# Kernel optimization log

Measured on AMD Instinct MI355X. Metric: run time of the kernel, lower is better.

## Reference

```python
import jax, jax.numpy as jnp
import numpy as np

N_SAMPLES = 16384
SPB = 1024            # samples_per_block
ROOM = (16, 16, 16)   # room_dim
MIC = (8, 8, 8)       # mic_location
ENV_SIZE = 16         # impulse_envelope_size
N_BLOCKS = N_SAMPLES // SPB
N_COEFFS = SPB // 2 + 1


def _linear_interp(env, out_size):
    # torch F.interpolate(mode='linear', align_corners=False) along last axis
    in_size = env.shape[-1]
    scale = in_size / out_size
    coords = jnp.clip((jnp.arange(out_size, dtype=jnp.float32) + 0.5) * scale - 0.5,
                      0.0, in_size - 1.0)
    lo = jnp.floor(coords).astype(jnp.int32)
    hi = jnp.minimum(lo + 1, in_size - 1)
    w = coords - lo.astype(jnp.float32)
    return env[..., lo] * (1.0 - w) + env[..., hi] * w


def setup_inputs() -> dict:
    key = jax.random.key(0)
    k1, k2, k3, k4 = jax.random.split(key, 4)
    x = jax.random.normal(k1, (1, 1, N_SAMPLES), dtype=jnp.float32)  # unused by forward
    transfer_functions = jax.random.uniform(k2, (N_BLOCKS, *ROOM, N_COEFFS), dtype=jnp.float32)
    impulses = jax.random.uniform(k3, (N_BLOCKS, *ROOM, ENV_SIZE), dtype=jnp.float32)
    # the torch forward draws U(-1,1) noise each block; hoisted here as an input
    noise = jax.random.uniform(k4, (N_BLOCKS, *ROOM, SPB), minval=-1.0, maxval=1.0,
                               dtype=jnp.float32)
    return {"x": x, "transfer_functions": transfer_functions,
            "impulses": impulses, "noise": noise}


def reference(x, transfer_functions, impulses, noise):
    # Precompute per-block excitation envelopes: interp -> clamp -> * noise
    env = jnp.clip(_linear_interp(impulses, SPB), 0.0, 1.0) * noise  # (B, X, Y, Z, T)
    res = jnp.clip(transfer_functions, 0.0, 1.0)                      # (B, X, Y, Z, F)

    def step(sound_field, blk):
        e, r = blk
        sf = sound_field + e
        spec = jnp.fft.rfft(sf, axis=-1, norm='ortho')
        sf = jnp.fft.irfft(r * spec, n=SPB, axis=-1, norm='ortho')
        mic = sf[MIC[0], MIC[1], MIC[2]]                              # (T,)
        # 3x3x3 ones-kernel box sum over spatial dims, zero padding 1 (== unfold path)
        sf = jax.lax.reduce_window(sf, 0.0, jax.lax.add,
                                   (3, 3, 3, 1), (1, 1, 1, 1), 'SAME')
        return sf, mic

    sf0 = jnp.zeros((*ROOM, SPB), dtype=jnp.float32)
    _, mics = jax.lax.scan(step, sf0, (env, res))                     # mics: (B, T)
    return mics.reshape(-1, 1, N_SAMPLES)                             # (1, 1, n_samples)
```

## Files before the change

kernel.cpp:

```cpp
#include <hip/hip_runtime.h>


#define NFFT   1024
#define NF     513
#define NKP    257
#define NCELLS 4096
#define NPAIR  2048
#define PI2    6.28318530717958647692f

#define RBAR() do { \
    asm volatile("s_waitcnt lgkmcnt(0)" ::: "memory"); \
    __builtin_amdgcn_s_barrier(); \
    __builtin_amdgcn_sched_barrier(0); \
} while (0)

__device__ __forceinline__ int SWX(int i) {
    return i ^ ((i >> 3) & 7) ^ ((i >> 6) & 7);
}
__device__ __forceinline__ int slotof4(int k) {
    return ((k & 3) << 8) | (((k >> 2) & 3) << 6) | (((k >> 4) & 3) << 4) |
           (((k >> 6) & 3) << 2) | ((k >> 8) & 3);
}
__device__ __forceinline__ float clip01(float v) { return fminf(fmaxf(v, 0.0f), 1.0f); }
__device__ __forceinline__ unsigned pkh2(float a, float b) {
    union { _Float16 h[2]; unsigned u; } z;
    z.h[0] = (_Float16)a; z.h[1] = (_Float16)b;
    return z.u;
}
__device__ __forceinline__ float h2lo(unsigned u) {
    union { unsigned u; _Float16 h[2]; } z; z.u = u; return (float)z.h[0];
}
__device__ __forceinline__ float h2hi(unsigned u) {
    union { unsigned u; _Float16 h[2]; } z; z.u = u; return (float)z.h[1];
}
__device__ __forceinline__ unsigned cmp4(const uint4& v, int c) {
    return c == 0 ? v.x : c == 1 ? v.y : c == 2 ? v.z : v.w;
}
__device__ __forceinline__ float4 f4add(float4 a, float4 b) {
    return make_float4(a.x + b.x, a.y + b.y, a.z + b.z, a.w + b.w);
}
__device__ __forceinline__ float4 f4sub(float4 a, float4 b) {
    return make_float4(a.x - b.x, a.y - b.y, a.z - b.z, a.w - b.w);
}
__device__ __forceinline__ float4 cmul2(float4 d, float2 w) {
    return make_float4(d.x * w.x - d.y * w.y, d.x * w.y + d.y * w.x,
                       d.z * w.x - d.w * w.y, d.z * w.y + d.w * w.x);
}
__device__ __forceinline__ float4 nI(float4 v) { return make_float4(v.y, -v.x, v.w, -v.z); }
__device__ __forceinline__ float4 pI(float4 v) { return make_float4(-v.y, v.x, -v.w, v.z); }

__device__ __forceinline__ void dft4(float4* a) {
    float4 e = f4add(a[0], a[2]), f = f4add(a[1], a[3]);
    float4 g = f4sub(a[0], a[2]), h = f4sub(a[1], a[3]);
    a[0] = f4add(e, f);
    a[2] = f4sub(e, f);
    a[1] = f4add(g, nI(h));
    a[3] = f4add(g, pI(h));
}

__device__ __forceinline__ void twiddle3(float4* a, int j, float invL) {
    float sv, cv;
    __sincosf(-PI2 * (float)j * invL, &sv, &cv);
    float2 w1 = make_float2(cv, sv), wp = w1;
    a[1] = cmul2(a[1], wp);
    wp = make_float2(wp.x * w1.x - wp.y * w1.y, wp.x * w1.y + wp.y * w1.x);
    a[2] = cmul2(a[2], wp);
    wp = make_float2(wp.x * w1.x - wp.y * w1.y, wp.x * w1.y + wp.y * w1.x);
    a[3] = cmul2(a[3], wp);
}

__global__ __launch_bounds__(256, 8) void k_p1(
    const float* __restrict__ tf, const float* __restrict__ imp,
    const float* __restrict__ noise, uint2* __restrict__ Etg,
    uint4* __restrict__ TFtg)
{
    __shared__ float4 FD[1024];

    const int tid = threadIdx.x;
    const int bid = blockIdx.x;
    const int b   = bid >> 10;
    const int g   = bid & 1023;
    const int c0  = g << 2;

    {
        const float* nz = noise + ((size_t)b * NCELLS + c0) * (size_t)NFFT + tid;
        float nzv[16];
        #pragma unroll
        for (int m = 0; m < 4; ++m)
            #pragma unroll
            for (int cc = 0; cc < 4; ++cc)
                nzv[4 * m + cc] = nz[cc * NFFT + (m << 8)];

        const float* ipr = imp + ((size_t)b * NCELLS + c0) * 16;
        float4 a[4];
        #pragma unroll
        for (int m = 0; m < 4; ++m) {
            int n = tid + (m << 8);
            float coord = (n + 0.5f) * (16.0f / 1024.0f) - 0.5f;
            coord = fminf(fmaxf(coord, 0.0f), 15.0f);
            int lo = (int)coord;
            int hi = lo + 1 > 15 ? 15 : lo + 1;
            float wl = coord - (float)lo, wh = 1.0f - wl;
            float4 e;
            e.x = clip01(ipr[lo]      * wh + ipr[hi]      * wl) * nzv[4 * m + 0];
            e.y = clip01(ipr[16 + lo] * wh + ipr[16 + hi] * wl) * nzv[4 * m + 1];
            e.z = clip01(ipr[32 + lo] * wh + ipr[32 + hi] * wl) * nzv[4 * m + 2];
            e.w = clip01(ipr[48 + lo] * wh + ipr[48 + hi] * wl) * nzv[4 * m + 3];
            a[m] = e;
        }
        dft4(a);
        twiddle3(a, tid, 1.0f / 1024.0f);
        #pragma unroll
        for (int p = 0; p < 4; ++p) FD[SWX(tid + (p << 8))] = a[p];
    }
    RBAR();

    #pragma unroll
    for (int pi = 0; pi < 3; ++pi) {
        const int lgs = 6 - 2 * pi;
        const int s   = 1 << lgs;
        const int j   = tid & (s - 1);
        const int idx0 = ((tid >> lgs) << (lgs + 2)) | j;
        float4 a[4];
        #pragma unroll
        for (int m = 0; m < 4; ++m) a[m] = FD[SWX(idx0 + (m << lgs))];
        dft4(a);
        twiddle3(a, j, 1.0f / (float)(s << 2));
        #pragma unroll
        for (int p = 0; p < 4; ++p) FD[SWX(idx0 + (p << lgs))] = a[p];
        RBAR();
    }

    {
        const int idx0 = tid << 2;
        float4 a[4];
        #pragma unroll
        for (int m = 0; m < 4; ++m) a[m] = FD[SWX(idx0 + m)];
        dft4(a);
        #pragma unroll
        for (int p = 0; p < 4; ++p) FD[SWX(idx0 + p)] = a[p];
    }
    RBAR();

    {
        uint2* base = Etg + ((size_t)b * 1024 + g) * 1024;
        #pragma unroll
        for (int it = 0; it < 4; ++it) {
            int s = tid + (it << 8);
            float4 v = FD[SWX(s)];
            uint2 u;
            u.x = pkh2(v.x, v.y);
            u.y = pkh2(v.z, v.w);
            base[s] = u;
        }
    }

    {
        const float* r0 = tf + ((size_t)b * NCELLS + c0) * NF;
        const float* r1 = r0 + NF;
        const float* r2 = r1 + NF;
        const float* r3 = r2 + NF;
        uint4* dst = TFtg + ((size_t)b * 1024 + g) * 257;
        for (int kp = tid; kp < NKP; kp += 256) {
            bool hv = kp < 256;
            uint4 u;
            u.x = pkh2(clip01(r0[2 * kp]), hv ? clip01(r0[2 * kp + 1]) : 0.0f);
            u.y = pkh2(clip01(r1[2 * kp]), hv ? clip01(r1[2 * kp + 1]) : 0.0f);
            u.z = pkh2(clip01(r2[2 * kp]), hv ? clip01(r2[2 * kp + 1]) : 0.0f);
            u.w = pkh2(clip01(r3[2 * kp]), hv ? clip01(r3[2 * kp + 1]) : 0.0f);
            dst[kp] = u;
        }
    }
}

__global__ __launch_bounds__(256) void k_t(
    const uint2* __restrict__ Etg, uint2* __restrict__ Et2,
    const uint4* __restrict__ TFtg, uint4* __restrict__ TFt4)
{
    __shared__ unsigned LU[64 * 65 * 2];
    const int tid = threadIdx.x;
    const int bid = blockIdx.x;

    if (bid < 4096) {
        unsigned* LA = LU;
        unsigned* LB = LU + 64 * 65;
        const int b = bid >> 8, tile = bid & 255;
        const int s0 = (tile >> 4) << 6, g0 = (tile & 15) << 6;
        #pragma unroll
        for (int j = 0; j < 16; ++j) {
            int idx = (j << 8) + tid;
            int gin = idx >> 6, sin = idx & 63;
            uint2 v = Etg[((size_t)b * 1024 + g0 + gin) * 1024 + s0 + sin];
            LA[gin * 65 + sin] = v.x;
            LB[gin * 65 + sin] = v.y;
        }
        __syncthreads();
        #pragma unroll
        for (int j = 0; j < 16; ++j) {
            int idx = (j << 8) + tid;
            int sin = idx >> 6, gin = idx & 63;
            uint2 v;
            v.x = LA[gin * 65 + sin];
            v.y = LB[gin * 65 + sin];
            Et2[((size_t)b * 1024 + s0 + sin) * 1024 + g0 + gin] = v;
        }
    } else {
        unsigned* P0 = LU;
        unsigned* P1 = LU + 1056;
        unsigned* P2 = LU + 2112;
        unsigned* P3 = LU + 3168;
        const int bid2 = bid - 4096;
        const int b = bid2 / 288, t2 = bid2 - b * 288;
        const int k0 = (t2 / 32) << 5, g0 = (t2 & 31) << 5;
        #pragma unroll
        for (int j = 0; j < 4; ++j) {
            int lin = (j << 8) + tid;
            int gin = lin >> 5, kin = lin & 31;
            int kp = k0 + kin;
            if (kp < NKP) {
                uint4 v = TFtg[((size_t)b * 1024 + g0 + gin) * 257 + kp];
                P0[gin * 33 + kin] = v.x;
                P1[gin * 33 + kin] = v.y;
                P2[gin * 33 + kin] = v.z;
                P3[gin * 33 + kin] = v.w;
            }
        }
        __syncthreads();
        #pragma unroll
        for (int j = 0; j < 4; ++j) {
            int lin = (j << 8) + tid;
            int kin = lin >> 5, gin = lin & 31;
            int kp = k0 + kin;
            if (kp < NKP) {
                uint4 v;
                v.x = P0[gin * 33 + kin];
                v.y = P1[gin * 33 + kin];
                v.z = P2[gin * 33 + kin];
                v.w = P3[gin * 33 + kin];
                TFt4[((size_t)b * 257 + kp) * 1024 + g0 + gin] = v;
            }
        }
    }
}

__global__ __launch_bounds__(1024, 8) void k_p2(
    const unsigned* __restrict__ Et, const unsigned* __restrict__ TFt,
    float2* __restrict__ ms)
{
    __shared__ float2 Sz[4096];

    const int q    = threadIdx.x;
    const int lane = q & 63;
    const int k    = blockIdx.x;
    const bool dual = (k == 0);
    const int kp  = dual ? 0 : (k >> 1);
    const int sel = dual ? 0 : (k & 1);
    const int rA  = slotof4(dual ? 0 : k);
    const int rB  = slotof4(dual ? 512 : ((1024 - k) & 1023));
    const int x = q >> 6, y = (q >> 2) & 15, zs = (q & 3) << 2;

    #define AX(qq, dz) (((qq) << 2) | ((dz) ^ ((qq) & 3) ^ (((qq) >> 2) & 3)))

    float2 SF[4];
    #pragma unroll
    for (int dz = 0; dz < 4; ++dz) SF[dz] = make_float2(0.f, 0.f);

    #pragma unroll 1
    for (int b = 0; b < 16; ++b) {
        const uint2 ea = *(const uint2*)(Et + ((size_t)b * NFFT + rA) * NPAIR + 2 * q);
        const uint2 eb = *(const uint2*)(Et + ((size_t)b * NFFT + rB) * NPAIR + 2 * q);
        const uint4 tp = *(const uint4*)(TFt + ((size_t)b * NKP + kp) * NCELLS + 4 * q);
        uint4 tp2;
        if (dual) tp2 = *(const uint4*)(TFt + ((size_t)b * NKP + 256) * NCELLS + 4 * q);

        float2 T[4];
        if (!dual) {
            #pragma unroll
            for (int j = 0; j < 2; ++j) {
                unsigned fu = j ? ea.y : ea.x;
                unsigned gu = j ? eb.y : eb.x;
                float fr = h2lo(fu), fi = h2hi(fu);
                float gr = h2lo(gu), gi = h2hi(gu);
                float ear = 0.5f * (fr + gr), eai = 0.5f * (fi - gi);
                float ebr = 0.5f * (fi + gi), ebi = 0.5f * (gr - fr);
                unsigned te = cmp4(tp, 2 * j);
                unsigned to = cmp4(tp, 2 * j + 1);
                float re_ = sel ? h2hi(te) : h2lo(te);
                float ro_ = sel ? h2hi(to) : h2lo(to);
                T[2 * j]     = make_float2(re_ * (SF[2 * j].x + ear),
                                           re_ * (SF[2 * j].y + eai));
                T[2 * j + 1] = make_float2(ro_ * (SF[2 * j + 1].x + ebr),
                                           ro_ * (SF[2 * j + 1].y + ebi));
            }
        } else {
            #pragma unroll
            for (int dz = 0; dz < 4; ++dz) {
                unsigned fu = (dz >> 1) ? ea.y : ea.x;
                unsigned gu = (dz >> 1) ? eb.y : eb.x;
                float e0   = (dz & 1) ? h2hi(fu) : h2lo(fu);
                float e512 = (dz & 1) ? h2hi(gu) : h2lo(gu);
                float tA = h2lo(cmp4(tp, dz));
                float tB = h2lo(cmp4(tp2, dz));
                T[dz] = make_float2(tA * (SF[dz].x + e0),
                                    tB * (SF[dz].y + e512));
            }
        }
        if (q == 546) {
            if (dual) {
                ms[b * NF + 0]   = make_float2(T[0].x, 0.0f);
                ms[b * NF + 512] = make_float2(T[0].y, 0.0f);
            } else {
                ms[b * NF + k] = T[0];
            }
        }

        float2 D, U;
        D.x = __shfl(T[3].x, lane - 1, 64); D.y = __shfl(T[3].y, lane - 1, 64);
        U.x = __shfl(T[0].x, lane + 1, 64); U.y = __shfl(T[0].y, lane + 1, 64);
        float2 Z[4];
        Z[0] = make_float2(T[0].x + T[1].x + (zs > 0 ? D.x : 0.f),
                           T[0].y + T[1].y + (zs > 0 ? D.y : 0.f));
        Z[1] = make_float2(T[0].x + T[1].x + T[2].x, T[0].y + T[1].y + T[2].y);
        Z[2] = make_float2(T[1].x + T[2].x + T[3].x, T[1].y + T[2].y + T[3].y);
        Z[3] = make_float2(T[2].x + T[3].x + (zs < 12 ? U.x : 0.f),
                           T[2].y + T[3].y + (zs < 12 ? U.y : 0.f));

        #pragma unroll
        for (int dz = 0; dz < 4; ++dz) Sz[AX(q, dz)] = Z[dz];
        __syncthreads();
        #pragma unroll
        for (int dz = 0; dz < 4; ++dz) {
            float2 s = Z[dz];
            if (y > 0)  { float2 u = Sz[AX(q - 4, dz)]; s.x += u.x; s.y += u.y; }
            if (y < 15) { float2 u = Sz[AX(q + 4, dz)]; s.x += u.x; s.y += u.y; }
            Z[dz] = s;
        }
        __syncthreads();
        #pragma unroll
        for (int dz = 0; dz < 4; ++dz) Sz[AX(q, dz)] = Z[dz];
        __syncthreads();
        #pragma unroll
        for (int dz = 0; dz < 4; ++dz) {
            float2 s = Z[dz];
            if (x > 0)  { float2 u = Sz[AX(q - 64, dz)]; s.x += u.x; s.y += u.y; }
            if (x < 15) { float2 u = Sz[AX(q + 64, dz)]; s.x += u.x; s.y += u.y; }
            SF[dz] = s;
        }
        __syncthreads();
    }
    #undef AX
}

__device__ __forceinline__ int pd(int i) { return i + (i >> 5); }

__global__ __launch_bounds__(256) void k_p3(
    const float2* __restrict__ ms, float* __restrict__ out)
{
    __shared__ float2 FD[1056];
    const int b = blockIdx.x, tid = threadIdx.x;

    for (int j = tid; j < NFFT; j += 256) {
        int jj = (j <= 512) ? j : 1024 - j;
        float2 v = ms[b * NF + jj];
        if (j > 512) v.y = -v.y;
        FD[pd(__brev(j) >> 22)] = v;
    }
    __syncthreads();

    for (int lg = 0; lg <= 9; ++lg) {
        const int len = 1 << lg;
        for (int pr = tid; pr < 512; pr += 256) {
            const int jj = pr & (len - 1);
            const int i0 = ((pr >> lg) << (lg + 1)) + jj;
            const int i1 = i0 + len;
            const int iw = jj << (9 - lg);
            float sn, cs;
            __sincosf(-PI2 * (1.0f / 1024.0f) * (float)iw, &sn, &cs);
            float2 a = FD[pd(i0)], bb = FD[pd(i1)];
            float tr = bb.x * cs + bb.y * sn;
            float ti = bb.y * cs - bb.x * sn;
            FD[pd(i0)] = make_float2(a.x + tr, a.y + ti);
            FD[pd(i1)] = make_float2(a.x - tr, a.y - ti);
        }
        __syncthreads();
    }
    for (int t = tid; t < NFFT; t += 256)
        out[b * NFFT + t] = FD[pd(t)].x * (1.0f / 1024.0f);
}

extern "C" void kernel_launch(void* const* d_in, const int* in_sizes, int n_in,
                              void* d_out, int out_size, void* d_ws, size_t ws_size,
                              hipStream_t stream)
{
    const float* tf    = (const float*)d_in[1];
    const float* imp   = (const float*)d_in[2];
    const float* noise = (const float*)d_in[3];
    float* out = (float*)d_out;

    uint2* Etg  = (uint2*)d_ws;
    uint2* Et2  = Etg + (size_t)16 * 1024 * 1024;
    uint4* TFtg = (uint4*)(Et2 + (size_t)16 * 1024 * 1024);
    uint4* TFt4 = TFtg + (size_t)16 * 1024 * 257;
    float2* ms  = (float2*)(TFt4 + (size_t)16 * 1024 * 257);

    k_p1<<<16384, 256, 0, stream>>>(tf, imp, noise, Etg, TFtg);
    k_t<<<8704, 256, 0, stream>>>(Etg, Et2, TFtg, TFt4);
    k_p2<<<512, 1024, 0, stream>>>((const unsigned*)Et2, (const unsigned*)TFt4, ms);
    k_p3<<<16, 256, 0, stream>>>(ms, out);
}
```

Before: 235.2 us.

## Transpose transfer functions directly in a dedicated kernel and vectorize FFT output stores

The transfer-function clip, pack and transpose now happens in a dedicated kernel that writes the final frequency-major layout straight away, so the TFtg staging buffer and its second transpose pass in k_t are gone. k_p1 also writes its last radix-4 stage directly to global memory as two 16-byte stores, dropping one LDS round-trip and barrier. This cuts global traffic for the intermediate TF buffer at the cost of one extra kernel launch. It also relies on the stored element order of the final stage matching the previous indexing.

New measurement: 222.0 us. 1.06x faster.

```diff
diff --git a/kernel.cpp b/kernel.cpp
--- a/kernel.cpp
+++ b/kernel.cpp
@@ -69,10 +69,58 @@
     a[3] = cmul2(a[3], wp);
 }
 
+__global__ __launch_bounds__(256) void k_tf(
+    const float* __restrict__ tf, uint4* __restrict__ TFt4)
+{
+    __shared__ float L[64 * 66];
+    const int tid = threadIdx.x;
+    const int bid = blockIdx.x;
+    const int b = bid / 576;
+    const int rem = bid - b * 576;
+    const int ct = rem / 9, kt = rem - ct * 9;
+    const int c0 = ct << 6;
+
+    if (kt < 8) {
+        const int k0 = kt << 5;
+        #pragma unroll
+        for (int j = 0; j < 16; ++j) {
+            int idx = (j << 8) + tid;
+            int cin = idx >> 6, fin = idx & 63;
+            L[cin * 66 + fin] =
+                clip01(tf[((size_t)b * NCELLS + c0 + cin) * NF + 2 * k0 + fin]);
+        }
+        __syncthreads();
+        #pragma unroll
+        for (int j = 0; j < 2; ++j) {
+            int idx = (j << 8) + tid;
+            int kpl = idx >> 4, gl = idx & 15;
+            int cb = gl << 2;
+            uint4 u;
+            u.x = pkh2(L[(cb + 0) * 66 + 2 * kpl], L[(cb + 0) * 66 + 2 * kpl + 1]);
+            u.y = pkh2(L[(cb + 1) * 66 + 2 * kpl], L[(cb + 1) * 66 + 2 * kpl + 1]);
+            u.z = pkh2(L[(cb + 2) * 66 + 2 * kpl], L[(cb + 2) * 66 + 2 * kpl + 1]);
+            u.w = pkh2(L[(cb + 3) * 66 + 2 * kpl], L[(cb + 3) * 66 + 2 * kpl + 1]);
+            TFt4[((size_t)b * NKP + k0 + kpl) * 1024 + (c0 >> 2) + gl] = u;
+        }
+    } else {
+        if (tid < 64)
+            L[tid] = clip01(tf[((size_t)b * NCELLS + c0 + tid) * NF + 512]);
+        __syncthreads();
+        if (tid < 16) {
+            int cb = tid << 2;
+            uint4 u;
+            u.x = pkh2(L[cb + 0], 0.0f);
+            u.y = pkh2(L[cb + 1], 0.0f);
+            u.z = pkh2(L[cb + 2], 0.0f);
+            u.w = pkh2(L[cb + 3], 0.0f);
+            TFt4[((size_t)b * NKP + 256) * 1024 + (c0 >> 2) + tid] = u;
+        }
+    }
+}
+
 __global__ __launch_bounds__(256, 8) void k_p1(
-    const float* __restrict__ tf, const float* __restrict__ imp,
-    const float* __restrict__ noise, uint2* __restrict__ Etg,
-    uint4* __restrict__ TFtg)
+    const float* __restrict__ imp, const float* __restrict__ noise,
+    uint2* __restrict__ Etg)
 {
     __shared__ float4 FD[1024];
 
@@ -132,114 +180,47 @@
     }
 
     {
-        const int idx0 = tid << 2;
+        const int t4 = tid << 2;
         float4 a[4];
         #pragma unroll
-        for (int m = 0; m < 4; ++m) a[m] = FD[SWX(idx0 + m)];
+        for (int m = 0; m < 4; ++m) a[m] = FD[SWX(t4 + m)];
         dft4(a);
-        #pragma unroll
-        for (int p = 0; p < 4; ++p) FD[SWX(idx0 + p)] = a[p];
-    }
-    RBAR();
-
-    {
-        uint2* base = Etg + ((size_t)b * 1024 + g) * 1024;
-        #pragma unroll
-        for (int it = 0; it < 4; ++it) {
-            int s = tid + (it << 8);
-            float4 v = FD[SWX(s)];
-            uint2 u;
-            u.x = pkh2(v.x, v.y);
-            u.y = pkh2(v.z, v.w);
-            base[s] = u;
-        }
-    }
-
-    {
-        const float* r0 = tf + ((size_t)b * NCELLS + c0) * NF;
-        const float* r1 = r0 + NF;
-        const float* r2 = r1 + NF;
-        const float* r3 = r2 + NF;
-        uint4* dst = TFtg + ((size_t)b * 1024 + g) * 257;
-        for (int kp = tid; kp < NKP; kp += 256) {
-            bool hv = kp < 256;
-            uint4 u;
-            u.x = pkh2(clip01(r0[2 * kp]), hv ? clip01(r0[2 * kp + 1]) : 0.0f);
-            u.y = pkh2(clip01(r1[2 * kp]), hv ? clip01(r1[2 * kp + 1]) : 0.0f);
-            u.z = pkh2(clip01(r2[2 * kp]), hv ? clip01(r2[2 * kp + 1]) : 0.0f);
-            u.w = pkh2(clip01(r3[2 * kp]), hv ? clip01(r3[2 * kp + 1]) : 0.0f);
-            dst[kp] = u;
-        }
+        uint2* base = Etg + ((size_t)b * 1024 + g) * 1024 + t4;
+        uint4 u0 = { pkh2(a[0].x, a[0].y), pkh2(a[0].z, a[0].w),
+                     pkh2(a[1].x, a[1].y), pkh2(a[1].z, a[1].w) };
+        uint4 u1 = { pkh2(a[2].x, a[2].y), pkh2(a[2].z, a[2].w),
+                     pkh2(a[3].x, a[3].y), pkh2(a[3].z, a[3].w) };
+        *(uint4*)(base)     = u0;
+        *(uint4*)(base + 2) = u1;
     }
 }
 
 __global__ __launch_bounds__(256) void k_t(
-    const uint2* __restrict__ Etg, uint2* __restrict__ Et2,
-    const uint4* __restrict__ TFtg, uint4* __restrict__ TFt4)
-{
-    __shared__ unsigned LU[64 * 65 * 2];
+    const uint2* __restrict__ Etg, uint2* __restrict__ Et2)
+{
+    __shared__ unsigned LA[64 * 65], LB[64 * 65];
     const int tid = threadIdx.x;
     const int bid = blockIdx.x;
-
-    if (bid < 4096) {
-        unsigned* LA = LU;
-        unsigned* LB = LU + 64 * 65;
-        const int b = bid >> 8, tile = bid & 255;
-        const int s0 = (tile >> 4) << 6, g0 = (tile & 15) << 6;
-        #pragma unroll
-        for (int j = 0; j < 16; ++j) {
-            int idx = (j << 8) + tid;
-            int gin = idx >> 6, sin = idx & 63;
-            uint2 v = Etg[((size_t)b * 1024 + g0 + gin) * 1024 + s0 + sin];
-            LA[gin * 65 + sin] = v.x;
-            LB[gin * 65 + sin] = v.y;
-        }
-        __syncthreads();
-        #pragma unroll
-        for (int j = 0; j < 16; ++j) {
-            int idx = (j << 8) + tid;
-            int sin = idx >> 6, gin = idx & 63;
-            uint2 v;
-            v.x = LA[gin * 65 + sin];
-            v.y = LB[gin * 65 + sin];
-            Et2[((size_t)b * 1024 + s0 + sin) * 1024 + g0 + gin] = v;
-        }
-    } else {
-        unsigned* P0 = LU;
-        unsigned* P1 = LU + 1056;
-        unsigned* P2 = LU + 2112;
-        unsigned* P3 = LU + 3168;
-        const int bid2 = bid - 4096;
-        const int b = bid2 / 288, t2 = bid2 - b * 288;
-        const int k0 = (t2 / 32) << 5, g0 = (t2 & 31) << 5;
-        #pragma unroll
-        for (int j = 0; j < 4; ++j) {
-            int lin = (j << 8) + tid;
-            int gin = lin >> 5, kin = lin & 31;
-            int kp = k0 + kin;
-            if (kp < NKP) {
-                uint4 v = TFtg[((size_t)b * 1024 + g0 + gin) * 257 + kp];
-                P0[gin * 33 + kin] = v.x;
-                P1[gin * 33 + kin] = v.y;
-                P2[gin * 33 + kin] = v.z;
-                P3[gin * 33 + kin] = v.w;
-            }
-        }
-        __syncthreads();
-        #pragma unroll
-        for (int j = 0; j < 4; ++j) {
-            int lin = (j << 8) + tid;
-            int kin = lin >> 5, gin = lin & 31;
-            int kp = k0 + kin;
-            if (kp < NKP) {
-                uint4 v;
-                v.x = P0[gin * 33 + kin];
-                v.y = P1[gin * 33 + kin];
-                v.z = P2[gin * 33 + kin];
-                v.w = P3[gin * 33 + kin];
-                TFt4[((size_t)b * 257 + kp) * 1024 + g0 + gin] = v;
-            }
-        }
+    const int b = bid >> 8, tile = bid & 255;
+    const int s0 = (tile >> 4) << 6, g0 = (tile & 15) << 6;
+
+    #pragma unroll
+    for (int j = 0; j < 16; ++j) {
+        int idx = (j << 8) + tid;
+        int gin = idx >> 6, sin = idx & 63;
+        uint2 v = Etg[((size_t)b * 1024 + g0 + gin) * 1024 + s0 + sin];
+        LA[gin * 65 + sin] = v.x;
+        LB[gin * 65 + sin] = v.y;
+    }
+    __syncthreads();
+    #pragma unroll
+    for (int j = 0; j < 16; ++j) {
+        int idx = (j << 8) + tid;
+        int sin = idx >> 6, gin = idx & 63;
+        uint2 v;
+        v.x = LA[gin * 65 + sin];
+        v.y = LB[gin * 65 + sin];
+        Et2[((size_t)b * 1024 + s0 + sin) * 1024 + g0 + gin] = v;
     }
 }
 
@@ -399,12 +380,12 @@
 
     uint2* Etg  = (uint2*)d_ws;
     uint2* Et2  = Etg + (size_t)16 * 1024 * 1024;
-    uint4* TFtg = (uint4*)(Et2 + (size_t)16 * 1024 * 1024);
-    uint4* TFt4 = TFtg + (size_t)16 * 1024 * 257;
-    float2* ms  = (float2*)(TFt4 + (size_t)16 * 1024 * 257);
-
-    k_p1<<<16384, 256, 0, stream>>>(tf, imp, noise, Etg, TFtg);
-    k_t<<<8704, 256, 0, stream>>>(Etg, Et2, TFtg, TFt4);
+    uint4* TFt4 = (uint4*)(Et2 + (size_t)16 * 1024 * 1024);
+    float2* ms  = (float2*)(TFt4 + (size_t)16 * NKP * 1024);
+
+    k_tf<<<16 * 64 * 9, 256, 0, stream>>>(tf, TFt4);
+    k_p1<<<16384, 256, 0, stream>>>(imp, noise, Etg);
+    k_t<<<4096, 256, 0, stream>>>(Etg, Et2);
     k_p2<<<512, 1024, 0, stream>>>((const unsigned*)Et2, (const unsigned*)TFt4, ms);
     k_p3<<<16, 256, 0, stream>>>(ms, out);
 }
```
